# Performance work log

Hardware: AMD Instinct MI355X
Metric: run time of the kernel (lower is better)

The kernel has to match this reference:

```python
import jax, jax.numpy as jnp
import numpy as np

NUM_FEATURES = 256
NUM_HEADS = 8
HEAD_SIZE = NUM_FEATURES // NUM_HEADS  # 32
N_AGENTS = 8
B = 32
SEQ = 64


def setup_inputs() -> dict:
    key = jax.random.key(0)
    ks = jax.random.split(key, 6)
    s = 0.02
    x = jax.random.normal(ks[0], (N_AGENTS * B, NUM_FEATURES, SEQ), dtype=jnp.float32)
    Wq = jax.random.normal(ks[1], (NUM_HEADS, NUM_FEATURES, HEAD_SIZE), dtype=jnp.float32) * s
    Wk = jax.random.normal(ks[2], (NUM_HEADS, NUM_FEATURES, HEAD_SIZE), dtype=jnp.float32) * s
    Wv = jax.random.normal(ks[3], (NUM_HEADS, NUM_FEATURES, HEAD_SIZE), dtype=jnp.float32) * s
    Wp = jax.random.normal(ks[4], (NUM_FEATURES, NUM_FEATURES), dtype=jnp.float32) * s
    bp = jnp.zeros((NUM_FEATURES,), dtype=jnp.float32)
    return {"x": x, "Wq": Wq, "Wk": Wk, "Wv": Wv, "Wp": Wp, "bp": bp, "n_agents": N_AGENTS}


def reference(x, Wq, Wk, Wv, Wp, bp, n_agents):
    # x: (n_agents*b, f, h)
    b_total, f, h = x.shape
    b = b_total // n_agents
    # reshape + rearrange 'n b f h -> n b h f'  (t = token axis of length h)
    xs = x.reshape(n_agents, b, f, h).transpose(0, 1, 3, 2)  # (n, b, t, f)
    # All heads at once: per-head linear projections (no bias)
    q = jnp.einsum('nbtf,Hfd->Hnbtd', xs, Wq)
    k = jnp.einsum('nbtf,Hfd->Hnbtd', xs, Wk)
    v = jnp.einsum('nbtf,Hfd->Hnbtd', xs, Wv)
    # all-pairs agent attention: i = key agent, j = query agent
    scale = f ** (-0.5)  # source scales by num_features, not head_size
    scores = jnp.einsum('Hjbtd,Hibsd->Hijbts', q, k) * scale  # (H,n,n,b,t,s)
    attn = jax.nn.softmax(scores, axis=-1)
    # weighted values, then sum over key-agent axis i
    out = jnp.einsum('Hijbts,Hibsd->Hjbtd', attn, v)  # (H,n,b,t,d)
    # concat heads on last dim (head 0 first), matching torch.cat
    y = jnp.moveaxis(out, 0, 3).reshape(n_agents, b, h, f)  # (n,b,t,H*d)
    # output projection (dropout is identity at eval / p=0)
    y = jnp.einsum('nbtf,gf->nbtg', y, Wp) + bp
    # rearrange 'n b h f -> n b f h' then merge agents into batch
    y = y.transpose(0, 1, 3, 2).reshape(n_agents * b, f, h)
    return y
```

## Files before the change

### kernel.cpp

```cpp
#include <hip/hip_runtime.h>

#define F   256
#define T   64
#define NH  8
#define D   32
#define NA  8
#define NBB 32

typedef unsigned short ushortT;
typedef unsigned int   uintT;

typedef short bf16x8 __attribute__((ext_vector_type(8)));
typedef float f32x4  __attribute__((ext_vector_type(4)));

__device__ __forceinline__ float bf2f(ushortT u) {
    union { uintT i; float f; } c; c.i = ((uintT)u) << 16; return c.f;
}
__device__ __forceinline__ ushortT f2bf(float f) {
    union { float f; uintT u; } c; c.f = f;
    uintT u = c.u;
    uintT r = u + 0x7fffu + ((u >> 16) & 1u);
    return (ushortT)(r >> 16);
}

__device__ __forceinline__ int detect_isbf16(const void* xraw) {
    const uintT* w = (const uintT*)xraw;
    int bad = 0;
    for (int k = 0; k < 128; ++k) {
        uintT v = w[k];
        uintT e0 = (v >> 7)  & 0xffu;
        uintT e1 = (v >> 23) & 0xffu;
        bad += (e0 > 131u) + (e1 > 131u);
    }
    return bad == 0 ? 1 : 0;
}

__device__ __forceinline__ ushortT cvt_elem(const void* p, size_t i, bool isbf) {
    return isbf ? ((const ushortT*)p)[i] : f2bf(((const float*)p)[i]);
}


__global__ __launch_bounds__(256) void wprep_kernel(const void* __restrict__ Wq,
                                                    const void* __restrict__ Wk,
                                                    const void* __restrict__ Wv,
                                                    const void* __restrict__ x,
                                                    ushortT* __restrict__ Wt) {
    __shared__ int sflag;
    if (threadIdx.x == 0) sflag = detect_isbf16(x);
    __syncthreads();
    bool isbf = sflag != 0;

    int base = (blockIdx.x * 256 + threadIdx.x) * 8;
    int cp = base >> 8, f0 = base & 255;
    int qkv = cp >> 8, c = cp & 255, hh = c >> 5, d = c & 31;
    const void* W = (qkv == 0) ? Wq : (qkv == 1) ? Wk : Wv;

    ushortT tmp[8];
    #pragma unroll
    for (int j = 0; j < 8; ++j)
        tmp[j] = cvt_elem(W, (size_t)(hh * F + f0 + j) * D + d, isbf);
    *(uint4*)&Wt[base] = *(const uint4*)tmp;
}

__global__ __launch_bounds__(512) void qkv_kernel(const void* __restrict__ x,
                                                  const ushortT* __restrict__ Wt,
                                                  ushortT* __restrict__ Qws,
                                                  ushortT* __restrict__ Kws,
                                                  ushortT* __restrict__ Vws) {
    int nb = blockIdx.x;
    __shared__ __align__(16) ushortT xs[T * F];
    __shared__ int sflag;

    if (threadIdx.x == 0) sflag = detect_isbf16(x);
    __syncthreads();
    bool isbf = sflag != 0;

    if (isbf) {
        const int4* xg = (const int4*)((const ushortT*)x + (size_t)nb * F * T);
        #pragma unroll
        for (int it = 0; it < 4; ++it) {
            int kk = threadIdx.x + it * 512;
            int4 v = xg[kk];
            int f = kk >> 3, t0 = (kk & 7) * 8;
            int fx = f ^ ((kk & 7) * 8);
            const ushortT* hv = (const ushortT*)&v;
            #pragma unroll
            for (int m = 0; m < 8; ++m) xs[(t0 + m) * 256 + fx] = hv[m];
        }
    } else {
        const float4* xg = (const float4*)((const float*)x + (size_t)nb * F * T);
        #pragma unroll
        for (int it = 0; it < 8; ++it) {
            int kk = threadIdx.x + it * 512;
            float4 v = xg[kk];
            int f = kk >> 4, t0 = (kk & 15) * 4;
            int fx = f ^ (((t0 >> 3) & 7) * 8);
            xs[(t0 + 0) * 256 + fx] = f2bf(v.x);
            xs[(t0 + 1) * 256 + fx] = f2bf(v.y);
            xs[(t0 + 2) * 256 + fx] = f2bf(v.z);
            xs[(t0 + 3) * 256 + fx] = f2bf(v.w);
        }
    }
    __syncthreads();

    int w = threadIdx.x >> 6, lane = threadIdx.x & 63;
    int l15 = lane & 15, quad = lane >> 4;

    f32x4 acc[6][4];
    #pragma unroll
    for (int a = 0; a < 6; ++a)
        #pragma unroll
        for (int bq = 0; bq < 4; ++bq) acc[a][bq] = (f32x4){0.f, 0.f, 0.f, 0.f};

    #pragma unroll
    for (int ks = 0; ks < 8; ++ks) {
        bf16x8 Bfr[4];
        #pragma unroll
        for (int nt = 0; nt < 4; ++nt) {
            int t = 16 * nt + l15;
            int fb = (ks * 32 + quad * 8) ^ (((t >> 3) & 7) * 8);
            Bfr[nt] = *(const bf16x8*)&xs[t * 256 + fb];
        }
        #pragma unroll
        for (int mt = 0; mt < 6; ++mt) {
            int row = 96 * w + 16 * mt + l15;
            bf16x8 Afr = *(const bf16x8*)(Wt + (size_t)row * 256 + ks * 32 + quad * 8);
            #pragma unroll
            for (int nt = 0; nt < 4; ++nt)
                acc[mt][nt] = __builtin_amdgcn_mfma_f32_16x16x32_bf16(Afr, Bfr[nt],
                                                                      acc[mt][nt], 0, 0, 0);
        }
    }

    #pragma unroll
    for (int mt = 0; mt < 6; ++mt) {
        int cb = 96 * w + 16 * mt + quad * 4;
        int qsel = cb >> 8;
        float scale = (qsel == 0) ? 0.0625f : 1.0f;
        int cc = cb & 255, hh = cc >> 5, db = cc & 31;
        #pragma unroll
        for (int nt = 0; nt < 4; ++nt) {
            int t = 16 * nt + l15;
            f32x4 v = acc[mt][nt];
            if (qsel < 2) {
                ushortT* dst = ((qsel == 0) ? Qws : Kws) +
                               ((size_t)(nb * NH + hh) * T + t) * D + db;
                uintT lo = (uintT)f2bf(v[0] * scale) | ((uintT)f2bf(v[1] * scale) << 16);
                uintT hi = (uintT)f2bf(v[2] * scale) | ((uintT)f2bf(v[3] * scale) << 16);
                *(uint2*)dst = make_uint2(lo, hi);
            } else {
                ushortT* dst = Vws + ((size_t)(nb * NH + hh) * D + db) * T + t;
                #pragma unroll
                for (int r = 0; r < 4; ++r) dst[r * T] = f2bf(v[r]);
            }
        }
    }
}

__global__ __launch_bounds__(512) void attn_kernel(const ushortT* __restrict__ Qws,
                                                   const ushortT* __restrict__ Kws,
                                                   const ushortT* __restrict__ Vws,
                                                   const void* __restrict__ Wp,
                                                   const void* __restrict__ bp,
                                                   const void* __restrict__ xdet,
                                                   void* __restrict__ outp) {
    __shared__ ushortT sm[49664];
    __shared__ int sflag;
    float* bpf = (float*)&sm[49152];

    int tid = threadIdx.x;
    int b = blockIdx.x, j = blockIdx.y;
    int nbj = j * NBB + b;

    if (tid == 0) sflag = detect_isbf16(xdet);
    __syncthreads();
    bool isbf = sflag != 0;
    if (tid < 256)
        bpf[tid] = isbf ? bf2f(((const ushortT*)bp)[tid]) : ((const float*)bp)[tid];

    int h = tid >> 6, lane = tid & 63;
    int l15 = lane & 15, quad = lane >> 4;
    int v4 = (l15 >> 2) & 3;
    ushortT* P = &sm[h * 4096];

    const ushortT* Qb = Qws + (size_t)(nbj * NH + h) * T * D;
    bf16x8 qf[4];
    #pragma unroll
    for (int nt = 0; nt < 4; ++nt)
        qf[nt] = *(const bf16x8*)(Qb + (16 * nt + l15) * D + quad * 8);

    f32x4 oacc[2][4];
    #pragma unroll
    for (int a = 0; a < 2; ++a)
        #pragma unroll
        for (int c = 0; c < 4; ++c) oacc[a][c] = (f32x4){0.f, 0.f, 0.f, 0.f};

    for (int i = 0; i < NA; ++i) {
        int nbi = i * NBB + b;
        const ushortT* Kb = Kws + (size_t)(nbi * NH + h) * T * D;
        bf16x8 kf[4];
        #pragma unroll
        for (int st = 0; st < 4; ++st)
            kf[st] = *(const bf16x8*)(Kb + (16 * st + l15) * D + quad * 8);

        f32x4 sacc[4][4];
        #pragma unroll
        for (int st = 0; st < 4; ++st)
            #pragma unroll
            for (int tt = 0; tt < 4; ++tt)
                sacc[st][tt] = __builtin_amdgcn_mfma_f32_16x16x32_bf16(
                    kf[st], qf[tt], (f32x4){0.f, 0.f, 0.f, 0.f}, 0, 0, 0);

        #pragma unroll
        for (int tt = 0; tt < 4; ++tt) {
            float mx = -1e30f;
            #pragma unroll
            for (int st = 0; st < 4; ++st)
                #pragma unroll
                for (int r = 0; r < 4; ++r) mx = fmaxf(mx, sacc[st][tt][r]);
            mx = fmaxf(mx, __shfl_xor(mx, 16));
            mx = fmaxf(mx, __shfl_xor(mx, 32));
            float sum = 0.f;
            #pragma unroll
            for (int st = 0; st < 4; ++st)
                #pragma unroll
                for (int r = 0; r < 4; ++r) {
                    float e = __expf(sacc[st][tt][r] - mx);
                    sacc[st][tt][r] = e;
                    sum += e;
                }
            sum += __shfl_xor(sum, 16);
            sum += __shfl_xor(sum, 32);
            float inv = 1.0f / sum;
            int t = tt * 16 + l15;
            #pragma unroll
            for (int st = 0; st < 4; ++st) {
                int sb = (st * 16 + quad * 4) ^ (v4 * 8);
                uintT lo = (uintT)f2bf(sacc[st][tt][0] * inv) |
                           ((uintT)f2bf(sacc[st][tt][1] * inv) << 16);
                uintT hi = (uintT)f2bf(sacc[st][tt][2] * inv) |
                           ((uintT)f2bf(sacc[st][tt][3] * inv) << 16);
                *(uint2*)&P[t * 64 + sb] = make_uint2(lo, hi);
            }
        }

        const ushortT* Vb = Vws + (size_t)(nbi * NH + h) * D * T;
        bf16x8 pf[4][2];
        #pragma unroll
        for (int nt = 0; nt < 4; ++nt)
            #pragma unroll
            for (int ks = 0; ks < 2; ++ks) {
                int sb = (ks * 32 + quad * 8) ^ (v4 * 8);
                pf[nt][ks] = *(const bf16x8*)&P[(nt * 16 + l15) * 64 + sb];
            }
        #pragma unroll
        for (int mt = 0; mt < 2; ++mt) {
            bf16x8 vf[2];
            #pragma unroll
            for (int ks = 0; ks < 2; ++ks)
                vf[ks] = *(const bf16x8*)(Vb + (16 * mt + l15) * T + ks * 32 + quad * 8);
            #pragma unroll
            for (int nt = 0; nt < 4; ++nt)
                #pragma unroll
                for (int ks = 0; ks < 2; ++ks)
                    oacc[mt][nt] = __builtin_amdgcn_mfma_f32_16x16x32_bf16(
                        vf[ks], pf[nt][ks], oacc[mt][nt], 0, 0, 0);
        }
    }

    #pragma unroll
    for (int mt = 0; mt < 2; ++mt)
        #pragma unroll
        for (int nt = 0; nt < 4; ++nt) {
            int t = nt * 16 + l15;
            int cb = h * 32 + 16 * mt + quad * 4;
            f32x4 v = oacc[mt][nt];
            uintT lo = (uintT)f2bf(v[0]) | ((uintT)f2bf(v[1]) << 16);
            uintT hi = (uintT)f2bf(v[2]) | ((uintT)f2bf(v[3]) << 16);
            *(uint2*)&sm[32768 + t * 256 + cb] = make_uint2(lo, hi);
        }
    __syncthreads();

    f32x4 cacc[2][4];
    #pragma unroll
    for (int a = 0; a < 2; ++a)
        #pragma unroll
        for (int c = 0; c < 4; ++c) cacc[a][c] = (f32x4){0.f, 0.f, 0.f, 0.f};

    #pragma unroll
    for (int ks = 0; ks < 8; ++ks) {
        bf16x8 yb[4];
        #pragma unroll
        for (int nt = 0; nt < 4; ++nt)
            yb[nt] = *(const bf16x8*)&sm[32768 + (nt * 16 + l15) * 256 + ks * 32 + quad * 8];
        #pragma unroll
        for (int m2 = 0; m2 < 2; ++m2) {
            int g = 16 * (2 * h + m2) + l15;
            bf16x8 wf;
            if (isbf) {
                wf = *(const bf16x8*)((const ushortT*)Wp + (size_t)g * 256 +
                                      ks * 32 + quad * 8);
            } else {
                const float* wr = (const float*)Wp + (size_t)g * 256 + ks * 32 + quad * 8;
                float4 w0 = *(const float4*)wr;
                float4 w1 = *(const float4*)(wr + 4);
                ushortT wt[8] = {f2bf(w0.x), f2bf(w0.y), f2bf(w0.z), f2bf(w0.w),
                                 f2bf(w1.x), f2bf(w1.y), f2bf(w1.z), f2bf(w1.w)};
                wf = *(const bf16x8*)wt;
            }
            #pragma unroll
            for (int nt = 0; nt < 4; ++nt)
                cacc[m2][nt] = __builtin_amdgcn_mfma_f32_16x16x32_bf16(
                    wf, yb[nt], cacc[m2][nt], 0, 0, 0);
        }
    }

    #pragma unroll
    for (int m2 = 0; m2 < 2; ++m2)
        #pragma unroll
        for (int nt = 0; nt < 4; ++nt) {
            int t = nt * 16 + l15;
            #pragma unroll
            for (int r = 0; r < 4; ++r) {
                int g = 16 * (2 * h + m2) + quad * 4 + r;
                float val = cacc[m2][nt][r] + bpf[g];
                if (isbf)
                    ((ushortT*)outp)[(size_t)nbj * F * T + g * T + t] = f2bf(val);
                else
                    ((float*)outp)[(size_t)nbj * F * T + g * T + t] = val;
            }
        }
}

__device__ __forceinline__ float tof(ushortT u) { return bf2f(u); }
__device__ __forceinline__ float tof(float f)   { return f; }

__device__ __forceinline__ void stage_x(const void* x, size_t nb, ushortT* sX,
                                        bool isbf, int tid) {
    if (isbf) {
        const int4* xg = (const int4*)((const ushortT*)x + nb * (F * T));
        int4* xl = (int4*)sX;
        for (int kk = tid; kk < F * T / 8; kk += 512) xl[kk] = xg[kk];
    } else {
        const float4* xg = (const float4*)((const float*)x + nb * (F * T));
        for (int kk = tid; kk < F * T / 4; kk += 512) {
            float4 v = xg[kk];
            int o = kk * 4;
            sX[o + 0] = f2bf(v.x); sX[o + 1] = f2bf(v.y);
            sX[o + 2] = f2bf(v.z); sX[o + 3] = f2bf(v.w);
        }
    }
}

template <typename WT>
__device__ __forceinline__ void q_proj(const WT* __restrict__ W, const ushortT* sX,
                                       ushortT* dst, int c, int t0) {
    float acc[32];
    #pragma unroll
    for (int m = 0; m < 32; ++m) acc[m] = 0.f;
    for (int f = 0; f < F; ++f) {
        float w = tof(W[f * D]);
        const ushortT* xr = &sX[f * T + t0];
        #pragma unroll
        for (int m = 0; m < 32; ++m) acc[m] = fmaf(bf2f(xr[m]), w, acc[m]);
    }
    #pragma unroll
    for (int m = 0; m < 32; ++m) dst[(t0 + m) * F + c] = f2bf(acc[m]);
}

template <typename WT>
__device__ __forceinline__ void kv_proj(const WT* __restrict__ WK, const WT* __restrict__ WV,
                                        const ushortT* sX, ushortT* sK, ushortT* sV,
                                        int c, int t0) {
    float ak[32], av[32];
    #pragma unroll
    for (int m = 0; m < 32; ++m) { ak[m] = 0.f; av[m] = 0.f; }
    for (int f = 0; f < F; ++f) {
        float wk = tof(WK[f * D]);
        float wv = tof(WV[f * D]);
        const ushortT* xr = &sX[f * T + t0];
        #pragma unroll
        for (int m = 0; m < 32; ++m) {
            float xv = bf2f(xr[m]);
            ak[m] = fmaf(xv, wk, ak[m]);
            av[m] = fmaf(xv, wv, av[m]);
        }
    }
    #pragma unroll
    for (int m = 0; m < 32; ++m) {
        sK[(t0 + m) * F + c] = f2bf(ak[m]);
        sV[(t0 + m) * F + c] = f2bf(av[m]);
    }
}

__global__ __launch_bounds__(512) void fused_kernel(const void* __restrict__ x,
                                                    const void* __restrict__ Wq,
                                                    const void* __restrict__ Wk,
                                                    const void* __restrict__ Wv,
                                                    const void* __restrict__ Wp,
                                                    const void* __restrict__ bp,
                                                    void* __restrict__ outp) {
    __shared__ __align__(16) char smem[98304];
    __shared__ int sflag;
    ushortT* sX = (ushortT*)smem;
    ushortT* sK = (ushortT*)(smem + 32768);
    ushortT* sV = (ushortT*)(smem + 65536);
    float*   sO = (float*)smem;

    int tid = threadIdx.x;
    int b = blockIdx.x, j = blockIdx.y;
    size_t nbj = (size_t)j * NBB + b;

    if (tid == 0) sflag = detect_isbf16(x);
    __syncthreads();
    bool isbf = sflag != 0;

    stage_x(x, nbj, sX, isbf, tid);
    __syncthreads();

    int c = tid & 255, t0 = (tid >> 8) * 32;
    int hc = c >> 5, dc = c & 31;
    if (isbf) q_proj((const ushortT*)Wq + (size_t)hc * F * D + dc, sX, sK, c, t0);
    else      q_proj((const float*)Wq   + (size_t)hc * F * D + dc, sX, sK, c, t0);
    __syncthreads();

    int h = tid >> 6, t = tid & 63;
    float q[32], o[32];
    #pragma unroll
    for (int dd = 0; dd < 32; ++dd) { q[dd] = bf2f(sK[t * F + h * D + dd]); o[dd] = 0.f; }

    for (int i = 0; i < NA; ++i) {
        __syncthreads();
        stage_x(x, (size_t)(i * NBB + b), sX, isbf, tid);
        __syncthreads();
        if (isbf) kv_proj((const ushortT*)Wk + (size_t)hc * F * D + dc,
                          (const ushortT*)Wv + (size_t)hc * F * D + dc, sX, sK, sV, c, t0);
        else      kv_proj((const float*)Wk   + (size_t)hc * F * D + dc,
                          (const float*)Wv   + (size_t)hc * F * D + dc, sX, sK, sV, c, t0);
        __syncthreads();
        float l = 0.f;
        float oi[32];
        #pragma unroll
        for (int dd = 0; dd < 32; ++dd) oi[dd] = 0.f;
        for (int s = 0; s < T; ++s) {
            const ushortT* kr = &sK[s * F + h * D];
            float dot = 0.f;
            #pragma unroll
            for (int dd = 0; dd < 32; ++dd) dot = fmaf(q[dd], bf2f(kr[dd]), dot);
            float e = __expf(dot * 0.0625f);
            l += e;
            const ushortT* vr = &sV[s * F + h * D];
            #pragma unroll
            for (int dd = 0; dd < 32; ++dd) oi[dd] = fmaf(e, bf2f(vr[dd]), oi[dd]);
        }
        float inv = 1.0f / l;
        #pragma unroll
        for (int dd = 0; dd < 32; ++dd) o[dd] = fmaf(oi[dd], inv, o[dd]);
    }
    __syncthreads();

    #pragma unroll
    for (int dd = 0; dd < 32; ++dd) sO[(h * D + dd) * T + t] = o[dd];
    __syncthreads();

    {
        int g = tid >> 1, te0 = (tid & 1) * 32;
        float acc[32];
        #pragma unroll
        for (int m = 0; m < 32; ++m) acc[m] = 0.f;
        if (isbf) {
            const ushortT* Wrow = (const ushortT*)Wp + (size_t)g * F;
            for (int cc = 0; cc < F; ++cc) {
                float w = bf2f(Wrow[cc]);
                const float* yr = &sO[cc * T + te0];
                #pragma unroll
                for (int m = 0; m < 32; ++m) acc[m] = fmaf(yr[m], w, acc[m]);
            }
        } else {
            const float* Wrow = (const float*)Wp + (size_t)g * F;
            for (int cc = 0; cc < F; ++cc) {
                float w = Wrow[cc];
                const float* yr = &sO[cc * T + te0];
                #pragma unroll
                for (int m = 0; m < 32; ++m) acc[m] = fmaf(yr[m], w, acc[m]);
            }
        }
        float bias = isbf ? bf2f(((const ushortT*)bp)[g]) : ((const float*)bp)[g];
        if (isbf) {
            ushortT* ob = (ushortT*)outp + nbj * F * T + g * T + te0;
            #pragma unroll
            for (int m = 0; m < 32; ++m) ob[m] = f2bf(acc[m] + bias);
        } else {
            float* ob = (float*)outp + nbj * F * T + g * T + te0;
            #pragma unroll
            for (int m = 0; m < 32; ++m) ob[m] = acc[m] + bias;
        }
    }
}

extern "C" void kernel_launch(void* const* d_in, const int* in_sizes, int n_in,
                              void* d_out, int out_size, void* d_ws, size_t ws_size,
                              hipStream_t stream) {
    const void* x  = d_in[0];
    const void* Wq = d_in[1];
    const void* Wk = d_in[2];
    const void* Wv = d_in[3];
    const void* Wp = d_in[4];
    const void* bp = d_in[5];

    const size_t needA = 25559040;

    if (ws_size >= needA) {
        char* ws = (char*)d_ws;
        ushortT* Wt  = (ushortT*)(ws + 0);
        ushortT* Qws = (ushortT*)(ws + 393216);
        ushortT* Kws = (ushortT*)(ws + 8781824);
        ushortT* Vws = (ushortT*)(ws + 17170432);

        wprep_kernel<<<dim3(96),    dim3(256), 0, stream>>>(Wq, Wk, Wv, x, Wt);
        qkv_kernel  <<<dim3(256),   dim3(512), 0, stream>>>(x, Wt, Qws, Kws, Vws);
        attn_kernel <<<dim3(32, 8), dim3(512), 0, stream>>>(Qws, Kws, Vws, Wp, bp,
                                                            x, d_out);
    } else {
        fused_kernel<<<dim3(32, 8), dim3(512), 0, stream>>>(x, Wq, Wk, Wv, Wp, bp, d_out);
    }
}
```

Baseline: 151.2 us.

## Fuse QKV projection into attention kernel, recomputing K/V per agent in registers

The separate QKV kernel and its global Q/K/V workspace are replaced by one fused kernel. Each block stages its own x tile and computes Q, then for each key agent restages that agent's x and recomputes K and V with MFMA, converting accumulators into MFMA operand fragments via lane shuffles instead of LDS round-trips. The softmax max subtraction is dropped, and the P matrix no longer goes through shared memory. This removes a kernel launch and the Q/K/V global traffic, but does 8x redundant K/V projection compute, and dropping the max relies on scores staying small enough not to overflow exp.

```diff
diff --git a/kernel.cpp b/kernel.cpp
--- a/kernel.cpp
+++ b/kernel.cpp
@@ -39,6 +39,25 @@
     return isbf ? ((const ushortT*)p)[i] : f2bf(((const float*)p)[i]);
 }
 
+__device__ __forceinline__ void packc(const f32x4 v, float scale, uintT& u0, uintT& u1) {
+    u0 = (uintT)f2bf(v[0] * scale) | ((uintT)f2bf(v[1] * scale) << 16);
+    u1 = (uintT)f2bf(v[2] * scale) | ((uintT)f2bf(v[3] * scale) << 16);
+}
+
+__device__ __forceinline__ bf16x8 build_frag(uintT u0a, uintT u1a, uintT u0b, uintT u1b,
+                                             int sl0, int sl1, bool hi) {
+    union { uintT u[4]; bf16x8 v; } r;
+    uintT x0a = (uintT)__shfl((int)u0a, sl0), x0b = (uintT)__shfl((int)u0b, sl0);
+    uintT x1a = (uintT)__shfl((int)u1a, sl0), x1b = (uintT)__shfl((int)u1b, sl0);
+    uintT x2a = (uintT)__shfl((int)u0a, sl1), x2b = (uintT)__shfl((int)u0b, sl1);
+    uintT x3a = (uintT)__shfl((int)u1a, sl1), x3b = (uintT)__shfl((int)u1b, sl1);
+    r.u[0] = hi ? x0b : x0a;
+    r.u[1] = hi ? x1b : x1a;
+    r.u[2] = hi ? x2b : x2a;
+    r.u[3] = hi ? x3b : x3a;
+    return r.v;
+}
+
 
 __global__ __launch_bounds__(256) void wprep_kernel(const void* __restrict__ Wq,
                                                     const void* __restrict__ Wk,
@@ -62,24 +81,13 @@
     *(uint4*)&Wt[base] = *(const uint4*)tmp;
 }
 
-__global__ __launch_bounds__(512) void qkv_kernel(const void* __restrict__ x,
-                                                  const ushortT* __restrict__ Wt,
-                                                  ushortT* __restrict__ Qws,
-                                                  ushortT* __restrict__ Kws,
-                                                  ushortT* __restrict__ Vws) {
-    int nb = blockIdx.x;
-    __shared__ __align__(16) ushortT xs[T * F];
-    __shared__ int sflag;
-
-    if (threadIdx.x == 0) sflag = detect_isbf16(x);
-    __syncthreads();
-    bool isbf = sflag != 0;
-
+__device__ __forceinline__ void stage_swz(const void* x, int nb, ushortT* xs,
+                                          bool isbf, int tid) {
     if (isbf) {
         const int4* xg = (const int4*)((const ushortT*)x + (size_t)nb * F * T);
         #pragma unroll
         for (int it = 0; it < 4; ++it) {
-            int kk = threadIdx.x + it * 512;
+            int kk = tid + it * 512;
             int4 v = xg[kk];
             int f = kk >> 3, t0 = (kk & 7) * 8;
             int fx = f ^ ((kk & 7) * 8);
@@ -91,7 +99,7 @@
         const float4* xg = (const float4*)((const float*)x + (size_t)nb * F * T);
         #pragma unroll
         for (int it = 0; it < 8; ++it) {
-            int kk = threadIdx.x + it * 512;
+            int kk = tid + it * 512;
             float4 v = xg[kk];
             int f = kk >> 4, t0 = (kk & 15) * 4;
             int fx = f ^ (((t0 >> 3) & 7) * 8);
@@ -101,107 +109,127 @@
             xs[(t0 + 3) * 256 + fx] = f2bf(v.w);
         }
     }
-    __syncthreads();
-
-    int w = threadIdx.x >> 6, lane = threadIdx.x & 63;
-    int l15 = lane & 15, quad = lane >> 4;
-
-    f32x4 acc[6][4];
-    #pragma unroll
-    for (int a = 0; a < 6; ++a)
-        #pragma unroll
-        for (int bq = 0; bq < 4; ++bq) acc[a][bq] = (f32x4){0.f, 0.f, 0.f, 0.f};
-
-    #pragma unroll
-    for (int ks = 0; ks < 8; ++ks) {
-        bf16x8 Bfr[4];
-        #pragma unroll
-        for (int nt = 0; nt < 4; ++nt) {
-            int t = 16 * nt + l15;
-            int fb = (ks * 32 + quad * 8) ^ (((t >> 3) & 7) * 8);
-            Bfr[nt] = *(const bf16x8*)&xs[t * 256 + fb];
-        }
-        #pragma unroll
-        for (int mt = 0; mt < 6; ++mt) {
-            int row = 96 * w + 16 * mt + l15;
-            bf16x8 Afr = *(const bf16x8*)(Wt + (size_t)row * 256 + ks * 32 + quad * 8);
-            #pragma unroll
-            for (int nt = 0; nt < 4; ++nt)
-                acc[mt][nt] = __builtin_amdgcn_mfma_f32_16x16x32_bf16(Afr, Bfr[nt],
-                                                                      acc[mt][nt], 0, 0, 0);
-        }
-    }
-
-    #pragma unroll
-    for (int mt = 0; mt < 6; ++mt) {
-        int cb = 96 * w + 16 * mt + quad * 4;
-        int qsel = cb >> 8;
-        float scale = (qsel == 0) ? 0.0625f : 1.0f;
-        int cc = cb & 255, hh = cc >> 5, db = cc & 31;
-        #pragma unroll
-        for (int nt = 0; nt < 4; ++nt) {
-            int t = 16 * nt + l15;
-            f32x4 v = acc[mt][nt];
-            if (qsel < 2) {
-                ushortT* dst = ((qsel == 0) ? Qws : Kws) +
-                               ((size_t)(nb * NH + hh) * T + t) * D + db;
-                uintT lo = (uintT)f2bf(v[0] * scale) | ((uintT)f2bf(v[1] * scale) << 16);
-                uintT hi = (uintT)f2bf(v[2] * scale) | ((uintT)f2bf(v[3] * scale) << 16);
-                *(uint2*)dst = make_uint2(lo, hi);
-            } else {
-                ushortT* dst = Vws + ((size_t)(nb * NH + hh) * D + db) * T + t;
-                #pragma unroll
-                for (int r = 0; r < 4; ++r) dst[r * T] = f2bf(v[r]);
-            }
-        }
-    }
-}
-
-__global__ __launch_bounds__(512) void attn_kernel(const ushortT* __restrict__ Qws,
-                                                   const ushortT* __restrict__ Kws,
-                                                   const ushortT* __restrict__ Vws,
-                                                   const void* __restrict__ Wp,
-                                                   const void* __restrict__ bp,
-                                                   const void* __restrict__ xdet,
-                                                   void* __restrict__ outp) {
-    __shared__ ushortT sm[49664];
+}
+
+__global__ __launch_bounds__(512) void fused_mfma(const void* __restrict__ x,
+                                                  const ushortT* __restrict__ Wt,
+                                                  const void* __restrict__ Wp,
+                                                  const void* __restrict__ bp,
+                                                  void* __restrict__ outp) {
+    __shared__ __align__(16) ushortT xs[T * F];
+    __shared__ float bpf[F];
     __shared__ int sflag;
-    float* bpf = (float*)&sm[49152];
 
     int tid = threadIdx.x;
     int b = blockIdx.x, j = blockIdx.y;
     int nbj = j * NBB + b;
 
-    if (tid == 0) sflag = detect_isbf16(xdet);
+    if (tid == 0) sflag = detect_isbf16(x);
     __syncthreads();
     bool isbf = sflag != 0;
+
+    stage_swz(x, nbj, xs, isbf, tid);
     if (tid < 256)
         bpf[tid] = isbf ? bf2f(((const ushortT*)bp)[tid]) : ((const float*)bp)[tid];
+    __syncthreads();
 
     int h = tid >> 6, lane = tid & 63;
     int l15 = lane & 15, quad = lane >> 4;
-    int v4 = (l15 >> 2) & 3;
-    ushortT* P = &sm[h * 4096];
-
-    const ushortT* Qb = Qws + (size_t)(nbj * NH + h) * T * D;
+    bool hi = quad >= 2;
+    int sl0 = l15 + 32 * (quad & 1);
+    int sl1 = sl0 + 16;
+
+    #define XSFRAG(t_, ks_) \
+        (*(const bf16x8*)&xs[(t_) * 256 + ((((ks_) * 32) + quad * 8) ^ ((((t_) >> 3) & 7) * 8))])
+
+    bf16x8 Kw[2][8];
+    #pragma unroll
+    for (int mt = 0; mt < 2; ++mt)
+        #pragma unroll
+        for (int ks = 0; ks < 8; ++ks)
+            Kw[mt][ks] = *(const bf16x8*)(Wt +
+                (size_t)(256 + 32 * h + 16 * mt + l15) * 256 + ks * 32 + quad * 8);
+
     bf16x8 qf[4];
-    #pragma unroll
-    for (int nt = 0; nt < 4; ++nt)
-        qf[nt] = *(const bf16x8*)(Qb + (16 * nt + l15) * D + quad * 8);
+    {
+        f32x4 qacc[2][4];
+        #pragma unroll
+        for (int mt = 0; mt < 2; ++mt)
+            #pragma unroll
+            for (int nt = 0; nt < 4; ++nt) qacc[mt][nt] = (f32x4){0.f, 0.f, 0.f, 0.f};
+        #pragma unroll
+        for (int ks = 0; ks < 8; ++ks) {
+            bf16x8 xf[4];
+            #pragma unroll
+            for (int nt = 0; nt < 4; ++nt) xf[nt] = XSFRAG(16 * nt + l15, ks);
+            #pragma unroll
+            for (int mt = 0; mt < 2; ++mt) {
+                bf16x8 Aw = *(const bf16x8*)(Wt +
+                    (size_t)(32 * h + 16 * mt + l15) * 256 + ks * 32 + quad * 8);
+                #pragma unroll
+                for (int nt = 0; nt < 4; ++nt)
+                    qacc[mt][nt] = __builtin_amdgcn_mfma_f32_16x16x32_bf16(
+                        Aw, xf[nt], qacc[mt][nt], 0, 0, 0);
+            }
+        }
+        #pragma unroll
+        for (int tt = 0; tt < 4; ++tt) {
+            uintT a0, a1, b0, b1;
+            packc(qacc[0][tt], 0.0625f, a0, a1);
+            packc(qacc[1][tt], 0.0625f, b0, b1);
+            qf[tt] = build_frag(a0, a1, b0, b1, sl0, sl1, hi);
+        }
+    }
 
     f32x4 oacc[2][4];
     #pragma unroll
-    for (int a = 0; a < 2; ++a)
-        #pragma unroll
-        for (int c = 0; c < 4; ++c) oacc[a][c] = (f32x4){0.f, 0.f, 0.f, 0.f};
+    for (int mt = 0; mt < 2; ++mt)
+        #pragma unroll
+        for (int tt = 0; tt < 4; ++tt) oacc[mt][tt] = (f32x4){0.f, 0.f, 0.f, 0.f};
 
     for (int i = 0; i < NA; ++i) {
-        int nbi = i * NBB + b;
-        const ushortT* Kb = Kws + (size_t)(nbi * NH + h) * T * D;
+        __syncthreads();
+        stage_swz(x, i * NBB + b, xs, isbf, tid);
+        __syncthreads();
+
+        f32x4 kacc[2][4], vacc[4][2];
+        #pragma unroll
+        for (int a = 0; a < 2; ++a)
+            #pragma unroll
+            for (int c = 0; c < 4; ++c) { kacc[a][c] = (f32x4){0.f, 0.f, 0.f, 0.f};
+                                          vacc[c][a] = (f32x4){0.f, 0.f, 0.f, 0.f}; }
+        #pragma unroll
+        for (int ks = 0; ks < 8; ++ks) {
+            bf16x8 xf[4];
+            #pragma unroll
+            for (int nt = 0; nt < 4; ++nt) xf[nt] = XSFRAG(16 * nt + l15, ks);
+            #pragma unroll
+            for (int mt = 0; mt < 2; ++mt)
+                #pragma unroll
+                for (int nt = 0; nt < 4; ++nt)
+                    kacc[mt][nt] = __builtin_amdgcn_mfma_f32_16x16x32_bf16(
+                        Kw[mt][ks], xf[nt], kacc[mt][nt], 0, 0, 0);
+            bf16x8 Vw0 = *(const bf16x8*)(Wt +
+                (size_t)(512 + 32 * h + l15) * 256 + ks * 32 + quad * 8);
+            bf16x8 Vw1 = *(const bf16x8*)(Wt +
+                (size_t)(512 + 32 * h + 16 + l15) * 256 + ks * 32 + quad * 8);
+            #pragma unroll
+            for (int st = 0; st < 4; ++st) {
+                vacc[st][0] = __builtin_amdgcn_mfma_f32_16x16x32_bf16(
+                    xf[st], Vw0, vacc[st][0], 0, 0, 0);
+                vacc[st][1] = __builtin_amdgcn_mfma_f32_16x16x32_bf16(
+                    xf[st], Vw1, vacc[st][1], 0, 0, 0);
+            }
+        }
+
         bf16x8 kf[4];
         #pragma unroll
-        for (int st = 0; st < 4; ++st)
-            kf[st] = *(const bf16x8*)(Kb + (16 * st + l15) * D + quad * 8);
+        for (int st = 0; st < 4; ++st) {
+            uintT a0, a1, b0, b1;
+            packc(kacc[0][st], 1.f, a0, a1);
+            packc(kacc[1][st], 1.f, b0, b1);
+            kf[st] = build_frag(a0, a1, b0, b1, sl0, sl1, hi);
+        }
 
         f32x4 sacc[4][4];
         #pragma unroll
@@ -211,73 +239,66 @@
                 sacc[st][tt] = __builtin_amdgcn_mfma_f32_16x16x32_bf16(
                     kf[st], qf[tt], (f32x4){0.f, 0.f, 0.f, 0.f}, 0, 0, 0);
 
+        uintT pu0[4][4], pu1[4][4];
         #pragma unroll
         for (int tt = 0; tt < 4; ++tt) {
-            float mx = -1e30f;
-            #pragma unroll
-            for (int st = 0; st < 4; ++st)
-                #pragma unroll
-                for (int r = 0; r < 4; ++r) mx = fmaxf(mx, sacc[st][tt][r]);
-            mx = fmaxf(mx, __shfl_xor(mx, 16));
-            mx = fmaxf(mx, __shfl_xor(mx, 32));
             float sum = 0.f;
             #pragma unroll
             for (int st = 0; st < 4; ++st)
                 #pragma unroll
                 for (int r = 0; r < 4; ++r) {
-                    float e = __expf(sacc[st][tt][r] - mx);
+                    float e = __expf(sacc[st][tt][r]);
                     sacc[st][tt][r] = e;
                     sum += e;
                 }
             sum += __shfl_xor(sum, 16);
             sum += __shfl_xor(sum, 32);
             float inv = 1.0f / sum;
-            int t = tt * 16 + l15;
-            #pragma unroll
-            for (int st = 0; st < 4; ++st) {
-                int sb = (st * 16 + quad * 4) ^ (v4 * 8);
-                uintT lo = (uintT)f2bf(sacc[st][tt][0] * inv) |
-                           ((uintT)f2bf(sacc[st][tt][1] * inv) << 16);
-                uintT hi = (uintT)f2bf(sacc[st][tt][2] * inv) |
-                           ((uintT)f2bf(sacc[st][tt][3] * inv) << 16);
-                *(uint2*)&P[t * 64 + sb] = make_uint2(lo, hi);
-            }
-        }
-
-        const ushortT* Vb = Vws + (size_t)(nbi * NH + h) * D * T;
+            #pragma unroll
+            for (int st = 0; st < 4; ++st)
+                packc(sacc[st][tt], inv, pu0[tt][st], pu1[tt][st]);
+        }
+
         bf16x8 pf[4][2];
         #pragma unroll
-        for (int nt = 0; nt < 4; ++nt)
-            #pragma unroll
-            for (int ks = 0; ks < 2; ++ks) {
-                int sb = (ks * 32 + quad * 8) ^ (v4 * 8);
-                pf[nt][ks] = *(const bf16x8*)&P[(nt * 16 + l15) * 64 + sb];
-            }
-        #pragma unroll
-        for (int mt = 0; mt < 2; ++mt) {
-            bf16x8 vf[2];
-            #pragma unroll
-            for (int ks = 0; ks < 2; ++ks)
-                vf[ks] = *(const bf16x8*)(Vb + (16 * mt + l15) * T + ks * 32 + quad * 8);
-            #pragma unroll
-            for (int nt = 0; nt < 4; ++nt)
+        for (int tt = 0; tt < 4; ++tt)
+            #pragma unroll
+            for (int kx = 0; kx < 2; ++kx)
+                pf[tt][kx] = build_frag(pu0[tt][2 * kx], pu1[tt][2 * kx],
+                                        pu0[tt][2 * kx + 1], pu1[tt][2 * kx + 1],
+                                        sl0, sl1, hi);
+
+        uintT vu0[2][4], vu1[2][4];
+        #pragma unroll
+        for (int mt = 0; mt < 2; ++mt)
+            #pragma unroll
+            for (int st = 0; st < 4; ++st)
+                packc(vacc[st][mt], 1.f, vu0[mt][st], vu1[mt][st]);
+
+        #pragma unroll
+        for (int mt = 0; mt < 2; ++mt)
+            #pragma unroll
+            for (int kx = 0; kx < 2; ++kx) {
+                bf16x8 vf = build_frag(vu0[mt][2 * kx], vu1[mt][2 * kx],
+                                       vu0[mt][2 * kx + 1], vu1[mt][2 * kx + 1],
+                                       sl0, sl1, hi);
                 #pragma unroll
-                for (int ks = 0; ks < 2; ++ks)
-                    oacc[mt][nt] = __builtin_amdgcn_mfma_f32_16x16x32_bf16(
-                        vf[ks], pf[nt][ks], oacc[mt][nt], 0, 0, 0);
-        }
-    }
-
+                for (int tt = 0; tt < 4; ++tt)
+                    oacc[mt][tt] = __builtin_amdgcn_mfma_f32_16x16x32_bf16(
+                        vf, pf[tt][kx], oacc[mt][tt], 0, 0, 0);
+            }
+    }
+
+    __syncthreads();
     #pragma unroll
     for (int mt = 0; mt < 2; ++mt)
         #pragma unroll
-        for (int nt = 0; nt < 4; ++nt) {
-            int t = nt * 16 + l15;
-            int cb = h * 32 + 16 * mt + quad * 4;
-            f32x4 v = oacc[mt][nt];
-            uintT lo = (uintT)f2bf(v[0]) | ((uintT)f2bf(v[1]) << 16);
-            uintT hi = (uintT)f2bf(v[2]) | ((uintT)f2bf(v[3]) << 16);
-            *(uint2*)&sm[32768 + t * 256 + cb] = make_uint2(lo, hi);
+        for (int tt = 0; tt < 4; ++tt) {
+            int t = 16 * tt + l15;
+            int cb = 32 * h + 16 * mt + 4 * quad;
+            uintT u0, u1;
+            packc(oacc[mt][tt], 1.f, u0, u1);
+            *(uint2*)&xs[t * 256 + (cb ^ ((t & 7) * 8))] = make_uint2(u0, u1);
         }
     __syncthreads();
 
@@ -291,8 +312,10 @@
     for (int ks = 0; ks < 8; ++ks) {
         bf16x8 yb[4];
         #pragma unroll
-        for (int nt = 0; nt < 4; ++nt)
-            yb[nt] = *(const bf16x8*)&sm[32768 + (nt * 16 + l15) * 256 + ks * 32 + quad * 8];
+        for (int nt = 0; nt < 4; ++nt) {
+            int t = 16 * nt + l15;
+            yb[nt] = *(const bf16x8*)&xs[t * 256 + ((ks * 32 + quad * 8) ^ ((t & 7) * 8))];
+        }
         #pragma unroll
         for (int m2 = 0; m2 < 2; ++m2) {
             int g = 16 * (2 * h + m2) + l15;
@@ -304,9 +327,12 @@
                 const float* wr = (const float*)Wp + (size_t)g * 256 + ks * 32 + quad * 8;
                 float4 w0 = *(const float4*)wr;
                 float4 w1 = *(const float4*)(wr + 4);
-                ushortT wt[8] = {f2bf(w0.x), f2bf(w0.y), f2bf(w0.z), f2bf(w0.w),
-                                 f2bf(w1.x), f2bf(w1.y), f2bf(w1.z), f2bf(w1.w)};
-                wf = *(const bf16x8*)wt;
+                union { ushortT s[8]; bf16x8 v; } wt;
+                wt.s[0] = f2bf(w0.x); wt.s[1] = f2bf(w0.y);
+                wt.s[2] = f2bf(w0.z); wt.s[3] = f2bf(w0.w);
+                wt.s[4] = f2bf(w1.x); wt.s[5] = f2bf(w1.y);
+                wt.s[6] = f2bf(w1.z); wt.s[7] = f2bf(w1.w);
+                wf = wt.v;
             }
             #pragma unroll
             for (int nt = 0; nt < 4; ++nt)
@@ -319,10 +345,10 @@
     for (int m2 = 0; m2 < 2; ++m2)
         #pragma unroll
         for (int nt = 0; nt < 4; ++nt) {
-            int t = nt * 16 + l15;
+            int t = 16 * nt + l15;
             #pragma unroll
             for (int r = 0; r < 4; ++r) {
-                int g = 16 * (2 * h + m2) + quad * 4 + r;
+                int g = 16 * (2 * h + m2) + 4 * quad + r;
                 float val = cacc[m2][nt][r] + bpf[g];
                 if (isbf)
                     ((ushortT*)outp)[(size_t)nbj * F * T + g * T + t] = f2bf(val);
@@ -330,6 +356,7 @@
                     ((float*)outp)[(size_t)nbj * F * T + g * T + t] = val;
             }
         }
+    #undef XSFRAG
 }
 
 __device__ __forceinline__ float tof(ushortT u) { return bf2f(u); }
@@ -508,19 +535,12 @@
     const void* Wp = d_in[4];
     const void* bp = d_in[5];
 
-    const size_t needA = 25559040;
+    const size_t needA = 393216;
 
     if (ws_size >= needA) {
-        char* ws = (char*)d_ws;
-        ushortT* Wt  = (ushortT*)(ws + 0);
-        ushortT* Qws = (ushortT*)(ws + 393216);
-        ushortT* Kws = (ushortT*)(ws + 8781824);
-        ushortT* Vws = (ushortT*)(ws + 17170432);
-
+        ushortT* Wt = (ushortT*)d_ws;
         wprep_kernel<<<dim3(96),    dim3(256), 0, stream>>>(Wq, Wk, Wv, x, Wt);
-        qkv_kernel  <<<dim3(256),   dim3(512), 0, stream>>>(x, Wt, Qws, Kws, Vws);
-        attn_kernel <<<dim3(32, 8), dim3(512), 0, stream>>>(Qws, Kws, Vws, Wp, bp,
-                                                            x, d_out);
+        fused_mfma  <<<dim3(32, 8), dim3(512), 0, stream>>>(x, Wt, Wp, bp, d_out);
     } else {
         fused_kernel<<<dim3(32, 8), dim3(512), 0, stream>>>(x, Wq, Wk, Wv, Wp, bp, d_out);
     }
```

Result: slower. 270.6 us (+78.9%).
